# Kernel optimization log

Hardware: AMD Instinct MI355X
Metric: run time of the kernel (lower is better)

The kernel has to match this reference:

```python
import jax, jax.numpy as jnp
import numpy as np

B, N, D = 2048, 64, 128
LRELU_ALPHA = 0.2
STEP = 2
NEG_BIG = -9e15


def _leaky(x):
    return jnp.where(x >= 0, x, LRELU_ALPHA * x)


def _local_agg(h, adj, a_list):
    # Original builds a_input[b,i,j,:] = h[b,i,:]*h[b,j,:] (O(N^2*D) buffer)
    # then e_k = leakyrelu(a_input @ a_k).  Mathematically e_k[b,i,j] =
    # leakyrelu(sum_d h[b,i,d]*a_k[d]*h[b,j,d]) = bilinear score, computed
    # here directly as a batched GEMM (same math, no N^2*D intermediate).
    logits = jnp.full(h.shape[:2] + (h.shape[1],), NEG_BIG, dtype=h.dtype)
    for k, a in enumerate(a_list):
        e_k = _leaky(jnp.einsum('bid,bjd->bij', h * a[:, 0], h))
        logits = jnp.where(adj == (k + 1), e_k, logits)
    att = jax.nn.softmax(logits, axis=-1)          # [B,N,N]
    return att @ h                                  # [B,N,D]


def setup_inputs() -> dict:
    key = jax.random.key(0)
    ks = jax.random.split(key, 13)
    hidden = jax.random.normal(ks[0], (B, N, D), dtype=jnp.float32)
    adj = jax.random.randint(ks[1], (B, N, N), 0, 5, dtype=jnp.int32)
    mask = (jax.random.uniform(ks[2], (B, N)) < 0.8).astype(jnp.float32)
    mask = mask.at[:, 0].set(1.0)  # guarantee at least one valid node per session
    s = 1.0 / np.sqrt(D)
    mk = lambda i, shp: (jax.random.normal(ks[i], shp, dtype=jnp.float32) * s)
    return {
        'hidden': hidden, 'adj': adj, 'mask': mask,
        'a_0': mk(3, (D, 1)), 'a_1': mk(4, (D, 1)),
        'a_2': mk(5, (D, 1)), 'a_3': mk(6, (D, 1)),
        'q_1': mk(7, (D, D)), 'k_1': mk(8, (D, D)),
        'q_2': mk(9, (D, D)), 'k_2': mk(10, (D, D)),
        'W_lin': mk(11, (D, 2 * D)),  # torch Linear(2D -> D, no bias) weight
    }


def reference(hidden, adj, mask, a_0, a_1, a_2, a_3,
              q_1, k_1, q_2, k_2, W_lin):
    sqrt_d = jnp.sqrt(jnp.asarray(D, hidden.dtype))
    # star init: masked mean over nodes -> [B,1,D]
    avg = jnp.sum(hidden * mask[..., None], axis=1) / jnp.sum(mask, axis=1, keepdims=True)
    star = avg[:, None, :]
    sate = hidden
    a_list = (a_0, a_1, a_2, a_3)
    for _ in range(STEP):
        sate = _local_agg(sate, adj, a_list)
        # satellite -> star attention (scalar gate per node)
        q = sate @ q_1                               # [B,N,D]
        k = star @ k_1                               # [B,1,D]
        alpha = (q @ jnp.swapaxes(k, -2, -1)) / sqrt_d  # [B,N,1]
        sate = (1.0 - alpha) * sate + alpha * star
        # star update: masked attention over satellites
        q2 = star @ q_2                              # [B,1,D]
        k2 = sate @ k_2                              # [B,N,D]
        beta = (q2 @ jnp.swapaxes(k2, -2, -1)) / sqrt_d  # [B,1,N]
        beta = jnp.where(mask[:, None, :] == 0, -jnp.inf, beta)
        beta = jax.nn.softmax(beta, axis=-1)
        star = beta @ sate                           # [B,1,D]
    gate = jax.nn.sigmoid(jnp.concatenate([hidden, sate], axis=-1) @ W_lin.T)
    out = gate * hidden + (1.0 - gate) * sate
    return out, star
```

## Files before the change

kernel.cpp:

```cpp
#include <hip/hip_runtime.h>

#define BDIM 256
constexpr int Bc = 2048;
constexpr int Nc = 64;
constexpr int Dc = 128;
constexpr float NEG_BIG_F = -9.0e15f;
constexpr float INV_SQRT_D = 0.08838834764831845f;

typedef __attribute__((ext_vector_type(8))) short bf16x8;
typedef __attribute__((ext_vector_type(4))) float f32x4;

#define MFMA16(A, B, C) __builtin_amdgcn_mfma_f32_16x16x32_bf16((A), (B), (C), 0, 0, 0)

__device__ __forceinline__ float bf2f(ushort u) {
    union { float f; unsigned int i; } cv;
    cv.i = ((unsigned int)u) << 16;
    return cv.f;
}
__device__ __forceinline__ ushort f2bf(float f) {
    union { float f; unsigned int i; } cv;
    cv.f = f;
    unsigned int x = cv.i;
    unsigned int r = (x >> 16) & 1u;
    x += 0x7fffu + r;
    return (ushort)(x >> 16);
}
__device__ __forceinline__ float rmax16(float v) {
#pragma unroll
    for (int off = 1; off < 16; off <<= 1) v = fmaxf(v, __shfl_xor(v, off, 64));
    return v;
}
__device__ __forceinline__ float rsum16(float v) {
#pragma unroll
    for (int off = 1; off < 16; off <<= 1) v += __shfl_xor(v, off, 64);
    return v;
}

__global__ __launch_bounds__(BDIM, 2) void star_agg_kernel(
    const float* __restrict__ hid,
    const int*   __restrict__ adj,
    const float* __restrict__ maskp,
    const float* __restrict__ a0p, const float* __restrict__ a1p,
    const float* __restrict__ a2p, const float* __restrict__ a3p,
    const float* __restrict__ q1p, const float* __restrict__ k1p,
    const float* __restrict__ q2p, const float* __restrict__ k2p,
    const float* __restrict__ wlp,
    float* __restrict__ outp)
{
    __shared__ __align__(16) ushort hb[Nc][136];
    __shared__ __align__(16) ushort hlo[Nc][136];
    __shared__ __align__(16) ushort hbT[Dc][72];
    __shared__ __align__(16) ushort Pb[Nc][72];
    __shared__ float aL[4][Dc];
    __shared__ float star_s[Dc];
    __shared__ float kk_s[Dc], qq_s[Dc];
    __shared__ float vv_s[Dc], ww_s[Dc];
    __shared__ float m_s[Nc];
    __shared__ float beta_s[Nc];
    __shared__ float star_part[4][Dc];
    __shared__ float Ssum[4];

    const int b      = blockIdx.x;
    const int tid    = threadIdx.x;
    const int lane   = tid & 63;
    const int wv     = tid >> 6;
    const int lane15 = lane & 15;
    const int quad   = lane >> 4;

    {
        const float4* hp4 = (const float4*)(hid + (size_t)b * (Nc * Dc));
        for (int idx = tid; idx < (Nc * Dc) / 4; idx += BDIM) {
            const int r = idx >> 5;
            const int c = (idx & 31) * 4;
            const float4 v = hp4[idx];
            ushort4 hi4, lo4;
            hi4.x = f2bf(v.x); lo4.x = f2bf(v.x - bf2f(hi4.x));
            hi4.y = f2bf(v.y); lo4.y = f2bf(v.y - bf2f(hi4.y));
            hi4.z = f2bf(v.z); lo4.z = f2bf(v.z - bf2f(hi4.z));
            hi4.w = f2bf(v.w); lo4.w = f2bf(v.w - bf2f(hi4.w));
            *(ushort4*)&hb[r][c]  = hi4;
            *(ushort4*)&hlo[r][c] = lo4;
            hbT[c + 0][r] = hi4.x;
            hbT[c + 1][r] = hi4.y;
            hbT[c + 2][r] = hi4.z;
            hbT[c + 3][r] = hi4.w;
        }
        if (tid < 128) {
            const int t = tid >> 5, c4 = tid & 31;
            const float* ap = (t == 0) ? a0p : (t == 1) ? a1p : (t == 2) ? a2p : a3p;
            *(float4*)&aL[t][c4 * 4] = *(const float4*)&ap[c4 * 4];
        }
        if (tid < Nc) m_s[tid] = maskp[b * Nc + tid];
    }
    __syncthreads();

    if (tid < Dc) {
        float s = 0.f, ms = 0.f;
        for (int i = 0; i < Nc; ++i) {
            const float hv = bf2f(hb[i][tid]) + bf2f(hlo[i][tid]);
            s = fmaf(hv, m_s[i], s);
            ms += m_s[i];
        }
        star_s[tid] = s / ms;
    }
    __syncthreads();

    float s2[8][4];

    for (int step = 0; step < 2; ++step) {
        if (tid < Dc) {
            const int c = tid;
            float s = 0.f;
            for (int d = 0; d < Dc; ++d) s = fmaf(star_s[d], k1p[d * Dc + c], s);
            kk_s[c] = s;
        } else {
            const int c = tid - Dc;
            float s = 0.f;
            for (int d = 0; d < Dc; ++d) s = fmaf(star_s[d], q2p[d * Dc + c], s);
            qq_s[c] = s;
        }
        __syncthreads();
        if (tid < Dc) {
            const int c = tid;
            float s = 0.f;
            for (int e4 = 0; e4 < Dc; e4 += 4) {
                const float4 qv = *(const float4*)&q1p[c * Dc + e4];
                s = fmaf(qv.w, kk_s[e4 + 3], fmaf(qv.z, kk_s[e4 + 2],
                    fmaf(qv.y, kk_s[e4 + 1], fmaf(qv.x, kk_s[e4], s))));
            }
            vv_s[c] = s * INV_SQRT_D;
        } else {
            const int c = tid - Dc;
            float s = 0.f;
            for (int e4 = 0; e4 < Dc; e4 += 4) {
                const float4 kv = *(const float4*)&k2p[c * Dc + e4];
                s = fmaf(kv.w, qq_s[e4 + 3], fmaf(kv.z, qq_s[e4 + 2],
                    fmaf(kv.y, qq_s[e4 + 1], fmaf(kv.x, qq_s[e4], s))));
            }
            ww_s[c] = s * INV_SQRT_D;
        }
        __syncthreads();

        f32x4 eacc[4][4];
#pragma unroll
        for (int t = 0; t < 4; ++t)
#pragma unroll
            for (int n = 0; n < 4; ++n) eacc[t][n] = (f32x4)0.f;

        const int arow = wv * 16 + lane15;
#pragma unroll
        for (int kc = 0; kc < 4; ++kc) {
            const int ko = kc * 32 + quad * 8;
            const bf16x8 hh = *(const bf16x8*)&hb[arow][ko];
            const bf16x8 hl = *(const bf16x8*)&hlo[arow][ko];
            float hx[8];
#pragma unroll
            for (int e = 0; e < 8; ++e)
                hx[e] = bf2f((ushort)hh[e]) + bf2f((ushort)hl[e]);
            bf16x8 Ahi[4], Alo[4];
#pragma unroll
            for (int t = 0; t < 4; ++t) {
                const float4 a0 = *(const float4*)&aL[t][ko];
                const float4 a1 = *(const float4*)&aL[t][ko + 4];
                const float av[8] = {a0.x, a0.y, a0.z, a0.w, a1.x, a1.y, a1.z, a1.w};
#pragma unroll
                for (int e = 0; e < 8; ++e) {
                    const float p = hx[e] * av[e];
                    const ushort ph = f2bf(p);
                    const ushort pl = f2bf(p - bf2f(ph));
                    Ahi[t][e] = (short)ph;
                    Alo[t][e] = (short)pl;
                }
            }
#pragma unroll
            for (int n = 0; n < 4; ++n) {
                const int brow = n * 16 + lane15;
                const bf16x8 Bh = *(const bf16x8*)&hb[brow][ko];
                const bf16x8 Bl = *(const bf16x8*)&hlo[brow][ko];
#pragma unroll
                for (int t = 0; t < 4; ++t) {
                    eacc[t][n] = MFMA16(Ahi[t], Bh, eacc[t][n]);
                    eacc[t][n] = MFMA16(Ahi[t], Bl, eacc[t][n]);
                    eacc[t][n] = MFMA16(Alo[t], Bh, eacc[t][n]);
                }
            }
        }

        float lg[4][4];
#pragma unroll
        for (int n = 0; n < 4; ++n) {
#pragma unroll
            for (int r = 0; r < 4; ++r) {
                const int i = wv * 16 + quad * 4 + r;
                const int j = n * 16 + lane15;
                const int t = adj[(size_t)b * 4096 + i * 64 + j];
                const float v0 = eacc[0][n][r], v1 = eacc[1][n][r];
                const float v2 = eacc[2][n][r], v3 = eacc[3][n][r];
                const float sel = (t == 1) ? v0 : (t == 2) ? v1 : (t == 3) ? v2 : v3;
                const float e = (t >= 1 && t <= 4) ? ((sel >= 0.f) ? sel : 0.2f * sel)
                                                   : NEG_BIG_F;
                lg[n][r] = e;
            }
        }

#pragma unroll
        for (int r = 0; r < 4; ++r) {
            float mx = fmaxf(fmaxf(lg[0][r], lg[1][r]), fmaxf(lg[2][r], lg[3][r]));
            mx = rmax16(mx);
            float pr[4], s = 0.f;
#pragma unroll
            for (int n = 0; n < 4; ++n) { pr[n] = __expf(lg[n][r] - mx); s += pr[n]; }
            s = rsum16(s);
            const float inv = 1.f / s;
            const int irow = wv * 16 + quad * 4 + r;
#pragma unroll
            for (int n = 0; n < 4; ++n)
                Pb[irow][n * 16 + lane15] = f2bf(pr[n] * inv);
        }

        f32x4 s1[8];
#pragma unroll
        for (int nd = 0; nd < 8; ++nd) s1[nd] = (f32x4)0.f;
#pragma unroll
        for (int kc2 = 0; kc2 < 2; ++kc2) {
            const int ko = kc2 * 32 + quad * 8;
            const bf16x8 Pa = *(const bf16x8*)&Pb[wv * 16 + lane15][ko];
#pragma unroll
            for (int nd = 0; nd < 8; ++nd) {
                const int dc = nd * 16 + lane15;
                const bf16x8 Bf = *(const bf16x8*)&hbT[dc][ko];
                s1[nd] = MFMA16(Pa, Bf, s1[nd]);
            }
        }

        float vvv[8], stv[8];
#pragma unroll
        for (int nt = 0; nt < 8; ++nt) {
            vvv[nt] = vv_s[nt * 16 + lane15];
            stv[nt] = star_s[nt * 16 + lane15];
        }
#pragma unroll
        for (int r = 0; r < 4; ++r) {
            float part = 0.f;
#pragma unroll
            for (int nt = 0; nt < 8; ++nt) part = fmaf(s1[nt][r], vvv[nt], part);
            const float al = rsum16(part);
#pragma unroll
            for (int nt = 0; nt < 8; ++nt)
                s2[nt][r] = (1.f - al) * s1[nt][r] + al * stv[nt];
        }

        float www[8];
#pragma unroll
        for (int nt = 0; nt < 8; ++nt) www[nt] = ww_s[nt * 16 + lane15];
        float bm[4];
#pragma unroll
        for (int r = 0; r < 4; ++r) {
            float part = 0.f;
#pragma unroll
            for (int nt = 0; nt < 8; ++nt) part = fmaf(s2[nt][r], www[nt], part);
            const float bj = rsum16(part);
            const int j = wv * 16 + quad * 4 + r;
            bm[r] = (m_s[j] == 0.f) ? NEG_BIG_F : bj;
            if (lane15 == 0) beta_s[j] = bm[r];
        }
        __syncthreads();

        {
            float mx = NEG_BIG_F;
#pragma unroll
            for (int j4 = 0; j4 < 16; ++j4) {
                const float4 bv = *(const float4*)&beta_s[j4 * 4];
                mx = fmaxf(mx, fmaxf(fmaxf(bv.x, bv.y), fmaxf(bv.z, bv.w)));
            }
            float p[4];
#pragma unroll
            for (int r = 0; r < 4; ++r) p[r] = __expf(bm[r] - mx);
            float part[8];
#pragma unroll
            for (int nt = 0; nt < 8; ++nt) {
                float v = 0.f;
#pragma unroll
                for (int r = 0; r < 4; ++r) v = fmaf(p[r], s2[nt][r], v);
                v += __shfl_xor(v, 16, 64);
                v += __shfl_xor(v, 32, 64);
                part[nt] = v;
            }
            if (lane < 16) {
#pragma unroll
                for (int nt = 0; nt < 8; ++nt)
                    star_part[wv][nt * 16 + lane15] = part[nt];
            }
            float pw = p[0] + p[1] + p[2] + p[3];
            pw += __shfl_xor(pw, 16, 64);
            pw += __shfl_xor(pw, 32, 64);
            if (lane == 0) Ssum[wv] = pw;

#pragma unroll
            for (int nt = 0; nt < 8; ++nt) {
#pragma unroll
                for (int r = 0; r < 4; ++r) {
                    const float v = s2[nt][r];
                    const ushort hi = f2bf(v);
                    const ushort lo = f2bf(v - bf2f(hi));
                    const int row = wv * 16 + quad * 4 + r;
                    const int c   = nt * 16 + lane15;
                    hb[row][c]  = hi;
                    hlo[row][c] = lo;
                    hbT[c][row] = hi;
                }
            }
        }
        __syncthreads();
        if (tid < Dc) {
            const float S = Ssum[0] + Ssum[1] + Ssum[2] + Ssum[3];
            const float tot = star_part[0][tid] + star_part[1][tid]
                            + star_part[2][tid] + star_part[3][tid];
            star_s[tid] = tot / S;
        }
        __syncthreads();
    }

    f32x4 g[8];
#pragma unroll
    for (int n = 0; n < 8; ++n) g[n] = (f32x4)0.f;
    const int arow_g = wv * 16 + lane15;
    const float* hrowA = hid + ((size_t)b * 64 + arow_g) * Dc;
#pragma unroll
    for (int kc = 0; kc < 8; ++kc) {
        bf16x8 Ah, Al;
        const bool has_lo = (kc >= 4);
        if (!has_lo) {
            const int co = kc * 32 + quad * 8;
            const float4 h0 = *(const float4*)&hrowA[co];
            const float4 h1 = *(const float4*)&hrowA[co + 4];
            const float hv[8] = {h0.x, h0.y, h0.z, h0.w, h1.x, h1.y, h1.z, h1.w};
#pragma unroll
            for (int e = 0; e < 8; ++e) Ah[e] = (short)f2bf(hv[e]);
        } else {
            const int co = (kc - 4) * 32 + quad * 8;
            Ah = *(const bf16x8*)&hb[arow_g][co];
            Al = *(const bf16x8*)&hlo[arow_g][co];
        }
#pragma unroll
        for (int n = 0; n < 8; ++n) {
            const int orow = n * 16 + lane15;
            const float* wr = wlp + orow * 256 + kc * 32 + quad * 8;
            const float4 w0 = *(const float4*)&wr[0];
            const float4 w1 = *(const float4*)&wr[4];
            const float wvv[8] = {w0.x, w0.y, w0.z, w0.w, w1.x, w1.y, w1.z, w1.w};
            bf16x8 Bf;
#pragma unroll
            for (int e = 0; e < 8; ++e) Bf[e] = (short)f2bf(wvv[e]);
            g[n] = MFMA16(Ah, Bf, g[n]);
            if (has_lo) g[n] = MFMA16(Al, Bf, g[n]);
        }
    }

#pragma unroll
    for (int n = 0; n < 8; ++n) {
#pragma unroll
        for (int r = 0; r < 4; ++r) {
            const int i = wv * 16 + quad * 4 + r;
            const int o = n * 16 + lane15;
            const float gg = 1.f / (1.f + __expf(-g[n][r]));
            const float hv = hid[((size_t)b * 64 + i) * Dc + o];
            outp[((size_t)b * 64 + i) * Dc + o] = gg * hv + (1.f - gg) * s2[n][r];
        }
    }
    if (tid < Dc)
        outp[(size_t)Bc * Nc * Dc + (size_t)b * Dc + tid] = star_s[tid];
}

extern "C" void kernel_launch(void* const* d_in, const int* in_sizes, int n_in,
                              void* d_out, int out_size, void* d_ws, size_t ws_size,
                              hipStream_t stream) {
    const float* hid  = (const float*)d_in[0];
    const int*   adj  = (const int*)d_in[1];
    const float* mask = (const float*)d_in[2];
    const float* a0   = (const float*)d_in[3];
    const float* a1   = (const float*)d_in[4];
    const float* a2   = (const float*)d_in[5];
    const float* a3   = (const float*)d_in[6];
    const float* q1   = (const float*)d_in[7];
    const float* k1   = (const float*)d_in[8];
    const float* q2   = (const float*)d_in[9];
    const float* k2   = (const float*)d_in[10];
    const float* wl   = (const float*)d_in[11];
    float* out = (float*)d_out;

    star_agg_kernel<<<Bc, BDIM, 0, stream>>>(hid, adj, mask, a0, a1, a2, a3,
                                             q1, k1, q2, k2, wl, out);
}
```

Before: 437.0 us.

## Drop transposed LDS copy, prefetch packed adjacency, vectorize star projections

Removes the hbT transposed bf16 buffer and instead gathers the B operand for the P·h MFMA with eight strided 16-bit LDS reads from hb. Adjacency values are loaded once before the step loop and packed into two 32-bit registers as 4-bit codes, replacing two rounds of global loads. The star projection matvecs are restructured to use float4 reads of the shared vector and multiple independent accumulators. This reduces LDS footprint and global traffic, which may help occupancy, but adds scalar LDS gathers and possible bank conflicts in the attention GEMM.

Result: slower. 574.9 us (+31.5%).

```diff
diff --git a/kernel.cpp b/kernel.cpp
--- a/kernel.cpp
+++ b/kernel.cpp
@@ -49,14 +49,13 @@
 {
     __shared__ __align__(16) ushort hb[Nc][136];
     __shared__ __align__(16) ushort hlo[Nc][136];
-    __shared__ __align__(16) ushort hbT[Dc][72];
     __shared__ __align__(16) ushort Pb[Nc][72];
-    __shared__ float aL[4][Dc];
-    __shared__ float star_s[Dc];
-    __shared__ float kk_s[Dc], qq_s[Dc];
-    __shared__ float vv_s[Dc], ww_s[Dc];
+    __shared__ __align__(16) float aL[4][Dc];
+    __shared__ __align__(16) float star_s[Dc];
+    __shared__ __align__(16) float kk_s[Dc], qq_s[Dc];
+    __shared__ __align__(16) float vv_s[Dc], ww_s[Dc];
     __shared__ float m_s[Nc];
-    __shared__ float beta_s[Nc];
+    __shared__ __align__(16) float beta_s[Nc];
     __shared__ float star_part[4][Dc];
     __shared__ float Ssum[4];
 
@@ -80,10 +79,6 @@
             hi4.w = f2bf(v.w); lo4.w = f2bf(v.w - bf2f(hi4.w));
             *(ushort4*)&hb[r][c]  = hi4;
             *(ushort4*)&hlo[r][c] = lo4;
-            hbT[c + 0][r] = hi4.x;
-            hbT[c + 1][r] = hi4.y;
-            hbT[c + 2][r] = hi4.z;
-            hbT[c + 3][r] = hi4.w;
         }
         if (tid < 128) {
             const int t = tid >> 5, c4 = tid & 31;
@@ -91,6 +86,22 @@
             *(float4*)&aL[t][c4 * 4] = *(const float4*)&ap[c4 * 4];
         }
         if (tid < Nc) m_s[tid] = maskp[b * Nc + tid];
+    }
+
+    unsigned int apack0 = 0u, apack1 = 0u;
+    {
+        const int* ab = adj + (size_t)b * 4096;
+#pragma unroll
+        for (int n = 0; n < 4; ++n)
+#pragma unroll
+            for (int r = 0; r < 4; ++r) {
+                const int i = wv * 16 + quad * 4 + r;
+                const int j = n * 16 + lane15;
+                const unsigned t = (unsigned)ab[i * 64 + j] & 15u;
+                const int idx = n * 4 + r;
+                if (idx < 8) apack0 |= t << (idx * 4);
+                else         apack1 |= t << ((idx - 8) * 4);
+            }
     }
     __syncthreads();
 
@@ -108,36 +119,42 @@
     float s2[8][4];
 
     for (int step = 0; step < 2; ++step) {
-        if (tid < Dc) {
-            const int c = tid;
-            float s = 0.f;
-            for (int d = 0; d < Dc; ++d) s = fmaf(star_s[d], k1p[d * Dc + c], s);
-            kk_s[c] = s;
-        } else {
-            const int c = tid - Dc;
-            float s = 0.f;
-            for (int d = 0; d < Dc; ++d) s = fmaf(star_s[d], q2p[d * Dc + c], s);
-            qq_s[c] = s;
+        {
+            const float* Wp = (tid < Dc) ? k1p : q2p;
+            const int c = tid & 127;
+            float a0 = 0.f, a1 = 0.f, a2 = 0.f, a3 = 0.f;
+            for (int d = 0; d < Dc; d += 4) {
+                const float4 sv = *(const float4*)&star_s[d];
+                a0 = fmaf(sv.x, Wp[(d + 0) * Dc + c], a0);
+                a1 = fmaf(sv.y, Wp[(d + 1) * Dc + c], a1);
+                a2 = fmaf(sv.z, Wp[(d + 2) * Dc + c], a2);
+                a3 = fmaf(sv.w, Wp[(d + 3) * Dc + c], a3);
+            }
+            const float res = (a0 + a1) + (a2 + a3);
+            if (tid < Dc) kk_s[c] = res; else qq_s[c] = res;
         }
         __syncthreads();
-        if (tid < Dc) {
-            const int c = tid;
-            float s = 0.f;
-            for (int e4 = 0; e4 < Dc; e4 += 4) {
-                const float4 qv = *(const float4*)&q1p[c * Dc + e4];
-                s = fmaf(qv.w, kk_s[e4 + 3], fmaf(qv.z, kk_s[e4 + 2],
-                    fmaf(qv.y, kk_s[e4 + 1], fmaf(qv.x, kk_s[e4], s))));
-            }
-            vv_s[c] = s * INV_SQRT_D;
-        } else {
-            const int c = tid - Dc;
-            float s = 0.f;
-            for (int e4 = 0; e4 < Dc; e4 += 4) {
-                const float4 kv = *(const float4*)&k2p[c * Dc + e4];
-                s = fmaf(kv.w, qq_s[e4 + 3], fmaf(kv.z, qq_s[e4 + 2],
-                    fmaf(kv.y, qq_s[e4 + 1], fmaf(kv.x, qq_s[e4], s))));
-            }
-            ww_s[c] = s * INV_SQRT_D;
+        {
+            const float* Wp = (tid < Dc) ? q1p : k2p;
+            const float* xp = (tid < Dc) ? kk_s : qq_s;
+            const int c = tid & 127;
+            float a0 = 0.f, a1 = 0.f, a2 = 0.f, a3 = 0.f;
+            for (int e = 0; e < Dc; e += 16) {
+                const float4 w0 = *(const float4*)&Wp[c * Dc + e];
+                const float4 w1 = *(const float4*)&Wp[c * Dc + e + 4];
+                const float4 w2 = *(const float4*)&Wp[c * Dc + e + 8];
+                const float4 w3 = *(const float4*)&Wp[c * Dc + e + 12];
+                const float4 x0 = *(const float4*)&xp[e];
+                const float4 x1 = *(const float4*)&xp[e + 4];
+                const float4 x2 = *(const float4*)&xp[e + 8];
+                const float4 x3 = *(const float4*)&xp[e + 12];
+                a0 = fmaf(w0.w, x0.w, fmaf(w0.z, x0.z, fmaf(w0.y, x0.y, fmaf(w0.x, x0.x, a0))));
+                a1 = fmaf(w1.w, x1.w, fmaf(w1.z, x1.z, fmaf(w1.y, x1.y, fmaf(w1.x, x1.x, a1))));
+                a2 = fmaf(w2.w, x2.w, fmaf(w2.z, x2.z, fmaf(w2.y, x2.y, fmaf(w2.x, x2.x, a2))));
+                a3 = fmaf(w3.w, x3.w, fmaf(w3.z, x3.z, fmaf(w3.y, x3.y, fmaf(w3.x, x3.x, a3))));
+            }
+            const float res = ((a0 + a1) + (a2 + a3)) * INV_SQRT_D;
+            if (tid < Dc) vv_s[c] = res; else ww_s[c] = res;
         }
         __syncthreads();
 
@@ -191,9 +208,9 @@
         for (int n = 0; n < 4; ++n) {
 #pragma unroll
             for (int r = 0; r < 4; ++r) {
-                const int i = wv * 16 + quad * 4 + r;
-                const int j = n * 16 + lane15;
-                const int t = adj[(size_t)b * 4096 + i * 64 + j];
+                const int idx = n * 4 + r;
+                const int t = (int)((idx < 8 ? (apack0 >> (idx * 4))
+                                             : (apack1 >> ((idx - 8) * 4))) & 15u);
                 const float v0 = eacc[0][n][r], v1 = eacc[1][n][r];
                 const float v2 = eacc[2][n][r], v3 = eacc[3][n][r];
                 const float sel = (t == 1) ? v0 : (t == 2) ? v1 : (t == 3) ? v2 : v3;
@@ -228,7 +245,9 @@
 #pragma unroll
             for (int nd = 0; nd < 8; ++nd) {
                 const int dc = nd * 16 + lane15;
-                const bf16x8 Bf = *(const bf16x8*)&hbT[dc][ko];
+                bf16x8 Bf;
+#pragma unroll
+                for (int jj = 0; jj < 8; ++jj) Bf[jj] = (short)hb[ko + jj][dc];
                 s1[nd] = MFMA16(Pa, Bf, s1[nd]);
             }
         }
@@ -307,7 +326,6 @@
                     const int c   = nt * 16 + lane15;
                     hb[row][c]  = hi;
                     hlo[row][c] = lo;
-                    hbT[c][row] = hi;
                 }
             }
         }
```
